# Kernel tuning notes

Hardware: AMD Instinct MI355X
Metric: run time of the kernel (lower is better)

Reference implementation:

```python
import jax, jax.numpy as jnp
import numpy as np

WINDOW = 5
PAD = (WINDOW - 1) // 2


def setup_inputs() -> dict:
    key = jax.random.key(0)
    k1, k2 = jax.random.split(key)
    pred = jax.random.uniform(k1, (8, 3, 512, 512), dtype=jnp.float32)
    gt = jax.random.uniform(k2, (8, 3, 512, 512), dtype=jnp.float32)
    return {"pred": pred, "gt": gt}


def reference(pred, gt):
    B, C, H, W = pred.shape
    # reflect-pad both images once
    pw = ((0, 0), (0, 0), (PAD, PAD), (PAD, PAD))
    pp = jnp.pad(pred, pw, mode="reflect")
    gp = jnp.pad(gt, pw, mode="reflect")
    p_ctr = pp[:, :, PAD:PAD + H, PAD:PAD + W]  # == pred
    g_ctr = gp[:, :, PAD:PAD + H, PAD:PAD + W]  # == gt
    # Fused: accumulate |census(pred) - census(gt)| per shifted compare,
    # never materializing the [B,C,H,W,window^2] census tensors.
    # (Original also cats a zeros plane first; it contributes 0 to the sum.)
    ham = jnp.zeros_like(pred)
    for i in range(WINDOW):
        for j in range(WINDOW):
            if i == PAD and j == PAD:
                continue
            p_cmp = (pp[:, :, i:i + H, j:j + W] < p_ctr).astype(pred.dtype)
            g_cmp = (gp[:, :, i:i + H, j:j + W] < g_ctr).astype(pred.dtype)
            ham = ham + jnp.abs(p_cmp - g_cmp)
    return jnp.mean(ham)
```

## Files before the change

kernel.cpp:

```cpp
#include <hip/hip_runtime.h>

#define IMG_H 512
#define IMG_W 512
#define N_IMG 24
#define NPIX (N_IMG * IMG_H * IMG_W)
#define ROWS_PB 8
#define SROWS 10
#define LDSW 520
#define RBLK (IMG_H / ROWS_PB)
#define BLOCK 256
#define NBLOCKS (N_IMG * RBLK)

__device__ __forceinline__ int reflect_b(int x) {
    int a = x < 0 ? -x : x;
    int b = 2 * IMG_H - 2 - a;
    return a < b ? a : b;
}

#define ROW_LD(K)                                                      \
    {                                                                  \
        const int r_ = sl4 + (K);                                      \
        const float4 a_ = *(const float4*)&lds[0][r_][c4];             \
        const float4 b_ = *(const float4*)&lds[0][r_][c4 + 4];         \
        pw[K][0] = a_.x; pw[K][1] = a_.y; pw[K][2] = a_.z; pw[K][3] = a_.w; \
        pw[K][4] = b_.x; pw[K][5] = b_.y; pw[K][6] = b_.z; pw[K][7] = b_.w; \
        const float4 c_ = *(const float4*)&lds[1][r_][c4];             \
        const float4 d_ = *(const float4*)&lds[1][r_][c4 + 4];         \
        gw[K][0] = c_.x; gw[K][1] = c_.y; gw[K][2] = c_.z; gw[K][3] = c_.w; \
        gw[K][4] = d_.x; gw[K][5] = d_.y; gw[K][6] = d_.z; gw[K][7] = d_.w; \
    }

#define DO_ROW(R)                                                              \
    {                                                                          \
        const float pc0 = pw[R][2], pc1 = pw[R][3],                            \
                    pc2 = pw[R][4], pc3 = pw[R][5];                            \
        const float gc0 = gw[R][2], gc1 = gw[R][3],                            \
                    gc2 = gw[R][4], gc3 = gw[R][5];                            \
        _Pragma("unroll")                                                      \
        for (int dx = 1; dx <= 2; ++dx) {                                      \
            c0 += (int)((pw[R][2 + dx] < pc0) != (gw[R][2 + dx] < gc0));       \
            c1 += (int)((pw[R][3 + dx] < pc1) != (gw[R][3 + dx] < gc1));       \
            c2 += (int)((pw[R][4 + dx] < pc2) != (gw[R][4 + dx] < gc2));       \
            c3 += (int)((pw[R][5 + dx] < pc3) != (gw[R][5 + dx] < gc3));       \
        }                                                                      \
        _Pragma("unroll")                                                      \
        for (int dy = 1; dy <= 2; ++dy) {                                      \
            const int row = (R) + dy;                                          \
            _Pragma("unroll")                                                  \
            for (int dx = 0; dx < 5; ++dx) {                                   \
                c0 += (int)((pw[row][0 + dx] < pc0) != (gw[row][0 + dx] < gc0)); \
                c1 += (int)((pw[row][1 + dx] < pc1) != (gw[row][1 + dx] < gc1)); \
                c2 += (int)((pw[row][2 + dx] < pc2) != (gw[row][2 + dx] < gc2)); \
                c3 += (int)((pw[row][3 + dx] < pc3) != (gw[row][3 + dx] < gc3)); \
            }                                                                  \
        }                                                                      \
    }

__global__ __launch_bounds__(BLOCK, 3) void census_main(
    const float* __restrict__ pred, const float* __restrict__ gt,
    unsigned int* __restrict__ ws)
{
    const int b   = blockIdx.x;
    const int n   = (b & 7) * (NBLOCKS / 8) + (b >> 3);
    const int img = n >> 6;
    const int rb  = n & (RBLK - 1);
    const int h0  = rb * ROWS_PB;

    const float* __restrict__ pimg = pred + (size_t)img * IMG_H * IMG_W;
    const float* __restrict__ gimg = gt   + (size_t)img * IMG_H * IMG_W;

    __shared__ float lds[2][SROWS][LDSW];

    {
        const int q  = threadIdx.x & 127;
        const int rg = threadIdx.x >> 7;
        #pragma unroll
        for (int i = 0; i < 5; ++i) {
            const int lr = rg + 2 * i;
            const int gy = reflect_b(h0 + lr);
            const float4 pv = *(const float4*)(pimg + (size_t)gy * IMG_W + 4 * q);
            const float4 gv = *(const float4*)(gimg + (size_t)gy * IMG_W + 4 * q);
            *(float2*)&lds[0][lr][2 + 4 * q] = make_float2(pv.x, pv.y);
            *(float2*)&lds[0][lr][4 + 4 * q] = make_float2(pv.z, pv.w);
            *(float2*)&lds[1][lr][2 + 4 * q] = make_float2(gv.x, gv.y);
            *(float2*)&lds[1][lr][4 + 4 * q] = make_float2(gv.z, gv.w);
        }
    }

    if (threadIdx.x < 80) {
        const int r = threadIdx.x >> 3;
        const int i = (threadIdx.x >> 2) & 1;
        const int c = threadIdx.x & 3;
        const int srccol = (c == 0) ? 2 : (c == 1) ? 1 : (c == 2) ? 510 : 509;
        const int dst    = (c == 0) ? 0 : (c == 1) ? 1 : (c == 2) ? 514 : 515;
        const int gy = reflect_b(h0 + r);
        const float* base = i ? gimg : pimg;
        lds[i][r][dst] = base[(size_t)gy * IMG_W + srccol];
    }
    __syncthreads();

    const int sc  = threadIdx.x & 127;
    const int sl  = threadIdx.x >> 7;
    const int c4  = 4 * sc;
    const int sl4 = 4 * sl;

    float pw[6][8], gw[6][8];
    int c0 = 0, c1 = 0, c2 = 0, c3 = 0;

    ROW_LD(0) ROW_LD(1) ROW_LD(2)
    DO_ROW(0)
    ROW_LD(3) DO_ROW(1)
    ROW_LD(4) DO_ROW(2)
    ROW_LD(5) DO_ROW(3)

    int cnt = (c0 + c1) + (c2 + c3);

    #pragma unroll
    for (int off = 32; off > 0; off >>= 1)
        cnt += __shfl_down(cnt, off, 64);

    __shared__ int wave_sums[BLOCK / 64];
    const int lane = threadIdx.x & 63;
    const int wid  = threadIdx.x >> 6;
    if (lane == 0) wave_sums[wid] = cnt;
    __syncthreads();

    if (threadIdx.x == 0) {
        ws[blockIdx.x] = (unsigned int)(wave_sums[0] + wave_sums[1] +
                                        wave_sums[2] + wave_sums[3]);
    }
}

__global__ __launch_bounds__(BLOCK, 1) void census_reduce(
    const unsigned int* __restrict__ ws, float* __restrict__ out)
{
    unsigned int s = 0;
    #pragma unroll
    for (int i = 0; i < NBLOCKS / BLOCK; ++i)
        s += ws[threadIdx.x + i * BLOCK];

    #pragma unroll
    for (int off = 32; off > 0; off >>= 1)
        s += __shfl_down(s, off, 64);

    __shared__ unsigned int wsum[BLOCK / 64];
    const int lane = threadIdx.x & 63;
    const int wid  = threadIdx.x >> 6;
    if (lane == 0) wsum[wid] = s;
    __syncthreads();

    if (threadIdx.x == 0) {
        unsigned int tot = wsum[0] + wsum[1] + wsum[2] + wsum[3];
        out[0] = (float)(2.0 * (double)tot / (double)NPIX);
    }
}

extern "C" void kernel_launch(void* const* d_in, const int* in_sizes, int n_in,
                              void* d_out, int out_size, void* d_ws, size_t ws_size,
                              hipStream_t stream) {
    const float* pred = (const float*)d_in[0];
    const float* gt   = (const float*)d_in[1];
    float* out        = (float*)d_out;
    unsigned int* ws  = (unsigned int*)d_ws;

    census_main<<<NBLOCKS, BLOCK, 0, stream>>>(pred, gt, ws);
    census_reduce<<<1, BLOCK, 0, stream>>>(ws, out);
}
```

Measured before the change: 91.54 us.

## Process two row tiles per block with prefetch of second tile during compute

Each block now handles 16 rows as two 8-row tiles, and the launch is halved to 768 blocks. The second tile's global loads are issued through inline asm before computing the first tile, then written to LDS after an explicit vmcnt wait. This overlaps memory latency with compute and amortizes block launch overhead. It costs extra registers for the prefetch buffers, which may reduce occupancy, and leaves fewer blocks to spread across CUs.

```diff
diff --git a/kernel.cpp b/kernel.cpp
--- a/kernel.cpp
+++ b/kernel.cpp
@@ -7,14 +7,23 @@
 #define ROWS_PB 8
 #define SROWS 10
 #define LDSW 520
-#define RBLK (IMG_H / ROWS_PB)
 #define BLOCK 256
-#define NBLOCKS (N_IMG * RBLK)
+#define NBLK 768
+
+#define VMWAIT(N)                                             \
+    asm volatile("s_waitcnt vmcnt(" #N ")" ::: "memory");     \
+    __builtin_amdgcn_sched_barrier(0)
 
 __device__ __forceinline__ int reflect_b(int x) {
     int a = x < 0 ? -x : x;
     int b = 2 * IMG_H - 2 - a;
     return a < b ? a : b;
+}
+
+__device__ __forceinline__ float4 gload4(const float* p) {
+    float4 r;
+    asm volatile("global_load_dwordx4 %0, %1, off" : "=v"(r) : "v"(p));
+    return r;
 }
 
 #define ROW_LD(K)                                                      \
@@ -56,48 +65,72 @@
         }                                                                      \
     }
 
+#define COMPUTE_TILE()                                                 \
+    {                                                                  \
+        ROW_LD(0) ROW_LD(1) ROW_LD(2)                                  \
+        DO_ROW(0)                                                      \
+        ROW_LD(3) DO_ROW(1)                                            \
+        ROW_LD(4) DO_ROW(2)                                            \
+        ROW_LD(5) DO_ROW(3)                                            \
+    }
+
 __global__ __launch_bounds__(BLOCK, 3) void census_main(
     const float* __restrict__ pred, const float* __restrict__ gt,
     unsigned int* __restrict__ ws)
 {
     const int b   = blockIdx.x;
-    const int n   = (b & 7) * (NBLOCKS / 8) + (b >> 3);
-    const int img = n >> 6;
-    const int rb  = n & (RBLK - 1);
-    const int h0  = rb * ROWS_PB;
+    const int n   = (b & 7) * (NBLK / 8) + (b >> 3);
+    const int img = n >> 5;
+    const int h0  = (n & 31) * (2 * ROWS_PB);
 
     const float* __restrict__ pimg = pred + (size_t)img * IMG_H * IMG_W;
     const float* __restrict__ gimg = gt   + (size_t)img * IMG_H * IMG_W;
 
     __shared__ float lds[2][SROWS][LDSW];
 
-    {
-        const int q  = threadIdx.x & 127;
-        const int rg = threadIdx.x >> 7;
-        #pragma unroll
-        for (int i = 0; i < 5; ++i) {
-            const int lr = rg + 2 * i;
-            const int gy = reflect_b(h0 + lr);
-            const float4 pv = *(const float4*)(pimg + (size_t)gy * IMG_W + 4 * q);
-            const float4 gv = *(const float4*)(gimg + (size_t)gy * IMG_W + 4 * q);
-            *(float2*)&lds[0][lr][2 + 4 * q] = make_float2(pv.x, pv.y);
-            *(float2*)&lds[0][lr][4 + 4 * q] = make_float2(pv.z, pv.w);
-            *(float2*)&lds[1][lr][2 + 4 * q] = make_float2(gv.x, gv.y);
-            *(float2*)&lds[1][lr][4 + 4 * q] = make_float2(gv.z, gv.w);
-        }
-    }
-
+    const int q  = threadIdx.x & 127;
+    const int rg = threadIdx.x >> 7;
+
+    #pragma unroll
+    for (int i = 0; i < 5; ++i) {
+        const int lr = rg + 2 * i;
+        const int gy = reflect_b(h0 + lr);
+        const float4 pv = *(const float4*)(pimg + (size_t)gy * IMG_W + 4 * q);
+        const float4 gv = *(const float4*)(gimg + (size_t)gy * IMG_W + 4 * q);
+        *(float2*)&lds[0][lr][2 + 4 * q] = make_float2(pv.x, pv.y);
+        *(float2*)&lds[0][lr][4 + 4 * q] = make_float2(pv.z, pv.w);
+        *(float2*)&lds[1][lr][2 + 4 * q] = make_float2(gv.x, gv.y);
+        *(float2*)&lds[1][lr][4 + 4 * q] = make_float2(gv.z, gv.w);
+    }
+    int hr = 0, hi = 0, hdst = 0, hsrc = 0;
     if (threadIdx.x < 80) {
-        const int r = threadIdx.x >> 3;
-        const int i = (threadIdx.x >> 2) & 1;
+        hr   = threadIdx.x >> 3;
+        hi   = (threadIdx.x >> 2) & 1;
         const int c = threadIdx.x & 3;
-        const int srccol = (c == 0) ? 2 : (c == 1) ? 1 : (c == 2) ? 510 : 509;
-        const int dst    = (c == 0) ? 0 : (c == 1) ? 1 : (c == 2) ? 514 : 515;
-        const int gy = reflect_b(h0 + r);
-        const float* base = i ? gimg : pimg;
-        lds[i][r][dst] = base[(size_t)gy * IMG_W + srccol];
-    }
-    __syncthreads();
+        hsrc = (c == 0) ? 2 : (c == 1) ? 1 : (c == 2) ? 510 : 509;
+        hdst = (c == 0) ? 0 : (c == 1) ? 1 : (c == 2) ? 514 : 515;
+        const int gy = reflect_b(h0 + hr);
+        const float* base = hi ? gimg : pimg;
+        lds[hi][hr][hdst] = base[(size_t)gy * IMG_W + hsrc];
+    }
+    __syncthreads();
+
+    const int h1 = h0 + ROWS_PB;
+    float4 ppf[5], gpf[5];
+    #pragma unroll
+    for (int i = 0; i < 5; ++i) {
+        const int lr = rg + 2 * i;
+        const int gy = reflect_b(h1 + lr);
+        ppf[i] = gload4(pimg + (size_t)gy * IMG_W + 4 * q);
+        gpf[i] = gload4(gimg + (size_t)gy * IMG_W + 4 * q);
+    }
+    float halo1 = 0.0f;
+    if (threadIdx.x < 80) {
+        const int gy = reflect_b(h1 + hr);
+        const float* base = hi ? gimg : pimg;
+        halo1 = base[(size_t)gy * IMG_W + hsrc];
+    }
+    __builtin_amdgcn_sched_barrier(0);
 
     const int sc  = threadIdx.x & 127;
     const int sl  = threadIdx.x >> 7;
@@ -106,12 +139,23 @@
 
     float pw[6][8], gw[6][8];
     int c0 = 0, c1 = 0, c2 = 0, c3 = 0;
-
-    ROW_LD(0) ROW_LD(1) ROW_LD(2)
-    DO_ROW(0)
-    ROW_LD(3) DO_ROW(1)
-    ROW_LD(4) DO_ROW(2)
-    ROW_LD(5) DO_ROW(3)
+    COMPUTE_TILE()
+
+    __syncthreads();
+
+    VMWAIT(0);
+    #pragma unroll
+    for (int i = 0; i < 5; ++i) {
+        const int lr = rg + 2 * i;
+        *(float2*)&lds[0][lr][2 + 4 * q] = make_float2(ppf[i].x, ppf[i].y);
+        *(float2*)&lds[0][lr][4 + 4 * q] = make_float2(ppf[i].z, ppf[i].w);
+        *(float2*)&lds[1][lr][2 + 4 * q] = make_float2(gpf[i].x, gpf[i].y);
+        *(float2*)&lds[1][lr][4 + 4 * q] = make_float2(gpf[i].z, gpf[i].w);
+    }
+    if (threadIdx.x < 80) lds[hi][hr][hdst] = halo1;
+    __syncthreads();
+
+    COMPUTE_TILE()
 
     int cnt = (c0 + c1) + (c2 + c3);
 
@@ -136,7 +180,7 @@
 {
     unsigned int s = 0;
     #pragma unroll
-    for (int i = 0; i < NBLOCKS / BLOCK; ++i)
+    for (int i = 0; i < NBLK / BLOCK; ++i)
         s += ws[threadIdx.x + i * BLOCK];
 
     #pragma unroll
@@ -163,6 +207,6 @@
     float* out        = (float*)d_out;
     unsigned int* ws  = (unsigned int*)d_ws;
 
-    census_main<<<NBLOCKS, BLOCK, 0, stream>>>(pred, gt, ws);
+    census_main<<<NBLK, BLOCK, 0, stream>>>(pred, gt, ws);
     census_reduce<<<1, BLOCK, 0, stream>>>(ws, out);
 }
```

Result: no change. 91.18 us (-0.4%).
